# Kernel tuning notes

Hardware: AMD Instinct MI355X
Metric: run time of the kernel (lower is better)

The kernel has to match this reference:

```python
import jax, jax.numpy as jnp
import numpy as np

T, H, W = 4, 16, 16
S = T * H * W          # 1024 flattened sequence length
C = 576                # embd_dim
NH = 8                 # n_head
DK = C // NH           # 72 per-head dim
L = 4                  # n_layer
B = 4                  # batch
PD = C // 3            # 192 per-axis pos-embed dim


def setup_inputs() -> dict:
    key = jax.random.key(0)
    ks = jax.random.split(key, 10)
    s = 1.0 / np.sqrt(C)
    return {
        "x": jax.random.normal(ks[0], (B, T, H, W, C), jnp.float32),
        "pos0": jax.random.normal(ks[1], (T, PD), jnp.float32) * 0.01,
        "pos1": jax.random.normal(ks[2], (H, PD), jnp.float32) * 0.01,
        "pos2": jax.random.normal(ks[3], (W, PD), jnp.float32) * 0.01,
        "ln1_g": jnp.ones((L, C), jnp.float32),
        "ln1_b": jnp.zeros((L, C), jnp.float32),
        "wq": jax.random.normal(ks[4], (L, C, C), jnp.float32) * s,
        "wk": jax.random.normal(ks[5], (L, C, C), jnp.float32) * s,
        "wv": jax.random.normal(ks[6], (L, C, C), jnp.float32) * s,
        "wo": jax.random.normal(ks[7], (L, C, C), jnp.float32) * (s / np.sqrt(L)),
        "wo_b": jnp.zeros((L, C), jnp.float32),
        "ln2_g": jnp.ones((L, C), jnp.float32),
        "ln2_b": jnp.zeros((L, C), jnp.float32),
        "w1": jax.random.normal(ks[8], (L, C, 4 * C), jnp.float32) * s,
        "b1": jnp.zeros((L, 4 * C), jnp.float32),
        "w2": jax.random.normal(ks[9], (L, 4 * C, C), jnp.float32) * (s / 2.0),
        "b2": jnp.zeros((L, C), jnp.float32),
    }


def _layernorm(x, g, b):
    # Faithful to the source: float32 math, and (1e-5 + rsqrt(var)) multiplier
    # (note: source adds eps to rsqrt, not to var -- replicated exactly).
    xf = x.astype(jnp.float32)
    mu = xf.mean(-1, keepdims=True)
    var = jnp.mean(jnp.square(xf - mu), -1, keepdims=True)
    y = (xf - mu) * (1e-5 + jax.lax.rsqrt(var)) * g + b
    return y.astype(x.dtype)


def _stack(x, pos0, pos1, pos2, ln1_g, ln1_b, wq, wk, wv, wo, wo_b,
           ln2_g, ln2_b, w1, b1, w2, b2):
    b = x.shape[0]
    xf = x.reshape(b, S, C)
    # right_shift (decode_step=None): shift flattened tokens right by one
    xf = jnp.pad(xf[:, :-1], ((0, 0), (1, 0), (0, 0)))
    # broadcast positional embedding, concat along channel
    pos = jnp.concatenate([
        jnp.broadcast_to(pos0[:, None, None, :], (T, H, W, PD)),
        jnp.broadcast_to(pos1[None, :, None, :], (T, H, W, PD)),
        jnp.broadcast_to(pos2[None, None, :, :], (T, H, W, PD)),
    ], axis=-1).reshape(S, C)
    xf = xf + pos

    causal = jnp.tril(jnp.ones((S, S), bool))
    scale = 1.0 / np.sqrt(DK)
    neg_inf = jnp.float32(-jnp.inf)

    for l in range(L):  # fixed small layer loop
        # --- causal full self-attention ---
        h = _layernorm(xf, ln1_g[l], ln1_b[l])
        q = (h @ wq[l]).reshape(b, S, NH, DK).transpose(0, 2, 1, 3)
        k = (h @ wk[l]).reshape(b, S, NH, DK).transpose(0, 2, 1, 3)
        v = (h @ wv[l]).reshape(b, S, NH, DK).transpose(0, 2, 1, 3)
        att = jnp.einsum('bhqd,bhkd->bhqk', q, k) * scale
        att = jnp.where(causal, att, neg_inf)
        att = jax.nn.softmax(att, axis=-1)
        a = jnp.einsum('bhqk,bhkd->bhqd', att, v)
        a = a.transpose(0, 2, 1, 3).reshape(b, S, C)
        xf = xf + a @ wo[l] + wo_b[l]
        # --- FFN with GeLU2: sigmoid(1.702*x)*x ---
        h = _layernorm(xf, ln2_g[l], ln2_b[l])
        h = h @ w1[l] + b1[l]
        h = jax.nn.sigmoid(1.702 * h) * h
        xf = xf + h @ w2[l] + b2[l]
    return xf.reshape(b, T, H, W, C)


def reference(x, pos0, pos1, pos2, ln1_g, ln1_b, wq, wk, wv, wo, wo_b,
              ln2_g, ln2_b, w1, b1, w2, b2):
    return _stack(x, pos0, pos1, pos2, ln1_g, ln1_b, wq, wk, wv, wo, wo_b,
                  ln2_g, ln2_b, w1, b1, w2, b2)
```

## Files before the change

### kernel.cpp

```cpp
#include <hip/hip_runtime.h>
#include <hip/hip_bf16.h>

typedef __hip_bfloat16 bf16;
using bf16x8 = __attribute__((ext_vector_type(8))) short;
using f32x4  = __attribute__((ext_vector_type(4))) float;

#define S_LEN 1024
#define CDIM  576
#define NHEAD 8
#define DKH   72
#define BATCH 4
#define MROWS 4096
#define FFDIM 2304
#define QKVN  1728

__device__ __forceinline__ void gload16(const void* g, void* l) {
  __builtin_amdgcn_global_load_lds(
      (const __attribute__((address_space(1))) unsigned int*)g,
      (__attribute__((address_space(3))) unsigned int*)l, 16, 0, 0);
}

__device__ __forceinline__ short f2bf_bits(float x) {
  unsigned int u = __float_as_uint(x);
  u += 0x7fffu + ((u >> 16) & 1u);
  return (short)(u >> 16);
}

__global__ __launch_bounds__(256) void transpose_cvt(
    const float* __restrict__ in, bf16* __restrict__ out, int K, int N,
    size_t in_ls, size_t out_ls) {
  __shared__ float tile[32][33];
  const float* inl = in + (size_t)blockIdx.z * in_ls;
  bf16* outl = out + (size_t)blockIdx.z * out_ls;
  int n0 = blockIdx.x * 32, k0 = blockIdx.y * 32;
  int tx = threadIdx.x & 31, ty = threadIdx.x >> 5;
#pragma unroll
  for (int i = 0; i < 32; i += 8)
    tile[ty + i][tx] = inl[(size_t)(k0 + ty + i) * N + (n0 + tx)];
  __syncthreads();
#pragma unroll
  for (int i = 0; i < 32; i += 8)
    outl[(size_t)(n0 + ty + i) * K + (k0 + tx)] = __float2bfloat16(tile[tx][ty + i]);
}

__global__ __launch_bounds__(256) void build_xf(
    const float* __restrict__ x, const float* __restrict__ p0,
    const float* __restrict__ p1, const float* __restrict__ p2,
    float* __restrict__ xf) {
  int idx = blockIdx.x * 256 + threadIdx.x;
  int c4 = idx % 144;
  int s  = (idx / 144) & (S_LEN - 1);
  int b  = idx / (144 * S_LEN);
  int c  = c4 * 4;
  int t = s >> 8, hh = (s >> 4) & 15, w = s & 15;
  float4 pv;
  if (c < 192)       pv = *(const float4*)&p0[t  * 192 + c];
  else if (c < 384)  pv = *(const float4*)&p1[hh * 192 + c - 192];
  else               pv = *(const float4*)&p2[w  * 192 + c - 384];
  float4 xv = make_float4(0.f, 0.f, 0.f, 0.f);
  if (s > 0) xv = *(const float4*)&x[((size_t)b * S_LEN + s - 1) * CDIM + c];
  float4 r = make_float4(xv.x + pv.x, xv.y + pv.y, xv.z + pv.z, xv.w + pv.w);
  *(float4*)&xf[((size_t)b * S_LEN + s) * CDIM + c] = r;
}

__global__ __launch_bounds__(256) void ln_kernel(
    const float* __restrict__ x, const float* __restrict__ g,
    const float* __restrict__ b, bf16* __restrict__ out) {
  int row  = blockIdx.x * 4 + (threadIdx.x >> 6);
  int lane = threadIdx.x & 63;
  const float* xr = x + (size_t)row * CDIM;
  float vals[9];
  float sum = 0.f;
#pragma unroll
  for (int i = 0; i < 9; i++) { vals[i] = xr[lane + 64 * i]; sum += vals[i]; }
#pragma unroll
  for (int o = 1; o < 64; o <<= 1) sum += __shfl_xor(sum, o);
  float mu = sum * (1.f / CDIM);
  float vs = 0.f;
#pragma unroll
  for (int i = 0; i < 9; i++) { float d = vals[i] - mu; vs += d * d; }
#pragma unroll
  for (int o = 1; o < 64; o <<= 1) vs += __shfl_xor(vs, o);
  float mult = 1e-5f + rsqrtf(vs * (1.f / CDIM));
  bf16* orow = out + (size_t)row * CDIM;
#pragma unroll
  for (int i = 0; i < 9; i++) {
    int c = lane + 64 * i;
    orow[c] = __float2bfloat16((vals[i] - mu) * mult * g[c] + b[c]);
  }
}

template <int BM, bool BIAS, bool RES, int ACT, bool OUTBF>
__global__ __launch_bounds__(256) void gemm3(
    const bf16* __restrict__ A, const bf16* __restrict__ Bt,
    const float* __restrict__ bias, const float* __restrict__ res,
    void* __restrict__ outp, int N, int K) {
  constexpr int MI = BM / 32;
  __shared__ short ldsA[BM][44];
  __shared__ short ldsB[64][44];
  const int tid = threadIdx.x, lane = tid & 63, wave = tid >> 6;
  const int lr = lane & 15, quad = lane >> 4;
  const int m0 = blockIdx.x * BM, n0 = blockIdx.y * 64;
  const int wm = (wave & 1) * (BM / 2), wn = (wave >> 1) * 32;
  f32x4 acc[MI][2] = {};
  const int arow = (BM == 128) ? (tid >> 1) : (tid >> 2);
  const int acol = (BM == 128) ? ((tid & 1) * 16) : ((tid & 3) * 8);
  const int brow = tid >> 2, bcol = (tid & 3) * 8;
  const short* Ag = (const short*)A  + (size_t)(m0 + arow) * K + acol;
  const short* Bg = (const short*)Bt + (size_t)(n0 + brow) * K + bcol;

  for (int k0 = 0; k0 < K; k0 += 32) {
    bf16x8 av0 = *(const bf16x8*)(Ag + k0);
    bf16x8 av1;
    if (BM == 128) av1 = *(const bf16x8*)(Ag + k0 + 8);
    bf16x8 bv = *(const bf16x8*)(Bg + k0);
    *(bf16x8*)&ldsA[arow][acol] = av0;
    if (BM == 128) *(bf16x8*)&ldsA[arow][acol + 8] = av1;
    *(bf16x8*)&ldsB[brow][bcol] = bv;
    __syncthreads();
    bf16x8 af[MI], bfv[2];
#pragma unroll
    for (int mi = 0; mi < MI; mi++)
      af[mi] = *(const bf16x8*)&ldsA[wm + mi * 16 + lr][quad * 8];
#pragma unroll
    for (int ni = 0; ni < 2; ni++)
      bfv[ni] = *(const bf16x8*)&ldsB[wn + ni * 16 + lr][quad * 8];
#pragma unroll
    for (int mi = 0; mi < MI; mi++)
#pragma unroll
      for (int ni = 0; ni < 2; ni++)
        acc[mi][ni] = __builtin_amdgcn_mfma_f32_16x16x32_bf16(af[mi], bfv[ni], acc[mi][ni], 0, 0, 0);
    __syncthreads();
  }

  float* fout = (float*)outp;
  bf16*  bout = (bf16*)outp;
#pragma unroll
  for (int mi = 0; mi < MI; mi++)
#pragma unroll
    for (int ni = 0; ni < 2; ni++) {
      int col = n0 + wn + ni * 16 + lr;
#pragma unroll
      for (int r = 0; r < 4; r++) {
        int row = m0 + wm + mi * 16 + quad * 4 + r;
        float v = acc[mi][ni][r];
        if (BIAS) v += bias[col];
        if (ACT == 1) v = v / (1.f + __expf(-1.702f * v));
        size_t idx = (size_t)row * N + col;
        if (RES) v += res[idx];
        if (OUTBF) bout[idx] = __float2bfloat16(v);
        else       fout[idx] = v;
      }
    }
}

__global__ __launch_bounds__(256) void attn_mfma(
    const bf16* __restrict__ qkv, bf16* __restrict__ a) {
  __shared__ short ldsK[12 * 512];
  __shared__ short ldsVt[80][104];
  __shared__ short ldsP[4 * 1024];
  const int bh = blockIdx.y, b = bh >> 3, h = bh & 7;
  const int tid = threadIdx.x, wave = tid >> 6, lane = tid & 63;
  const int lr = lane & 15, quad = lane >> 4;
  const int qt = 15 - (int)blockIdx.x;
  const float scale = 0.11785113019775793f;
  const int qcol = h * DKH, kcol = CDIM + h * DKH, vcol = 2 * CDIM + h * DKH;

  const int qrow = qt * 64 + wave * 16 + lr;
  const short* qg = (const short*)qkv + (size_t)(b * S_LEN + qrow) * QKVN + qcol;
  bf16x8 qfrag[3];
#pragma unroll
  for (int c = 0; c < 3; c++) {
    int d0 = c * 32 + quad * 8;
    bf16x8 z = {0, 0, 0, 0, 0, 0, 0, 0};
    qfrag[c] = (d0 < DKH) ? *(const bf16x8*)(qg + d0) : z;
  }
  f32x4 oacc[5] = {};
  float m[4], l[4];
#pragma unroll
  for (int r = 0; r < 4; r++) { m[r] = -1e30f; l[r] = 0.f; }

  for (int kt = 0; kt <= qt; kt++) {
    __syncthreads();
    {
      const short* kg = (const short*)qkv +
          (size_t)(b * S_LEN + kt * 64 + wave * 16 + lr) * QKVN + kcol + quad * 8;
#pragma unroll
      for (int c = 0; c < 3; c++)
        gload16(kg + c * 32, &ldsK[(wave * 3 + c) * 512]);
    }
    {
      int key = tid & 63, dgb = tid >> 6;
      const short* vg = (const short*)qkv + (size_t)(b * S_LEN + kt * 64 + key) * QKVN + vcol;
#pragma unroll
      for (int pass = 0; pass < 3; pass++) {
        int d0 = (dgb + pass * 4) * 8;
        if (d0 < 80) {
          bf16x8 vv = {0, 0, 0, 0, 0, 0, 0, 0};
          if (d0 < DKH) vv = *(const bf16x8*)(vg + d0);
#pragma unroll
          for (int j = 0; j < 8; j++) ldsVt[d0 + j][key] = vv[j];
        }
      }
    }
    __syncthreads();
    f32x4 sacc[4] = {};
#pragma unroll
    for (int nc = 0; nc < 4; nc++)
#pragma unroll
      for (int c = 0; c < 3; c++) {
        bf16x8 kf = *(const bf16x8*)&ldsK[(nc * 3 + c) * 512 + lane * 8];
        sacc[nc] = __builtin_amdgcn_mfma_f32_16x16x32_bf16(qfrag[c], kf, sacc[nc], 0, 0, 0);
      }
    float tmax[4];
#pragma unroll
    for (int r = 0; r < 4; r++) tmax[r] = -1e30f;
    bool diag = (kt == qt);
#pragma unroll
    for (int nc = 0; nc < 4; nc++)
#pragma unroll
      for (int r = 0; r < 4; r++) {
        float s = sacc[nc][r] * scale;
        if (diag && (nc * 16 + lr > wave * 16 + quad * 4 + r)) s = -1e30f;
        sacc[nc][r] = s;
        tmax[r] = fmaxf(tmax[r], s);
      }
#pragma unroll
    for (int r = 0; r < 4; r++) {
      tmax[r] = fmaxf(tmax[r], __shfl_xor(tmax[r], 1));
      tmax[r] = fmaxf(tmax[r], __shfl_xor(tmax[r], 2));
      tmax[r] = fmaxf(tmax[r], __shfl_xor(tmax[r], 4));
      tmax[r] = fmaxf(tmax[r], __shfl_xor(tmax[r], 8));
    }
    float alpha[4], psum[4];
#pragma unroll
    for (int r = 0; r < 4; r++) {
      float mn = fmaxf(m[r], tmax[r]);
      alpha[r] = __expf(m[r] - mn);
      m[r] = mn;
      psum[r] = 0.f;
    }
#pragma unroll
    for (int nc = 0; nc < 4; nc++)
#pragma unroll
      for (int r = 0; r < 4; r++) {
        float p = __expf(sacc[nc][r] - m[r]);
        psum[r] += p;
        int col = nc * 16 + lr;
        ldsP[wave * 1024 + (col >> 5) * 512 +
             (((col >> 3) & 3) * 16 + quad * 4 + r) * 8 + (col & 7)] = f2bf_bits(p);
      }
#pragma unroll
    for (int r = 0; r < 4; r++) {
      psum[r] += __shfl_xor(psum[r], 1);
      psum[r] += __shfl_xor(psum[r], 2);
      psum[r] += __shfl_xor(psum[r], 4);
      psum[r] += __shfl_xor(psum[r], 8);
      l[r] = l[r] * alpha[r] + psum[r];
    }
#pragma unroll
    for (int dc = 0; dc < 5; dc++)
#pragma unroll
      for (int r = 0; r < 4; r++) oacc[dc][r] *= alpha[r];
    __builtin_amdgcn_sched_barrier(0);
    bf16x8 pfrag[2];
#pragma unroll
    for (int kc = 0; kc < 2; kc++)
      pfrag[kc] = *(const bf16x8*)&ldsP[wave * 1024 + kc * 512 + lane * 8];
#pragma unroll
    for (int dc = 0; dc < 5; dc++)
#pragma unroll
      for (int kc = 0; kc < 2; kc++) {
        bf16x8 vf = *(const bf16x8*)&ldsVt[dc * 16 + lr][kc * 32 + quad * 8];
        oacc[dc] = __builtin_amdgcn_mfma_f32_16x16x32_bf16(pfrag[kc], vf, oacc[dc], 0, 0, 0);
      }
  }

#pragma unroll
  for (int dc = 0; dc < 5; dc++) {
    int d = dc * 16 + lr;
    if (d < DKH) {
#pragma unroll
      for (int r = 0; r < 4; r++) {
        int row = qt * 64 + wave * 16 + quad * 4 + r;
        float val = oacc[dc][r] / l[r];
        a[(size_t)(b * S_LEN + row) * CDIM + h * DKH + d] = __float2bfloat16(val);
      }
    }
  }
}

extern "C" void kernel_launch(void* const* d_in, const int* in_sizes, int n_in,
                              void* d_out, int out_size, void* d_ws, size_t ws_size,
                              hipStream_t stream) {
  const float* x    = (const float*)d_in[0];
  const float* pos0 = (const float*)d_in[1];
  const float* pos1 = (const float*)d_in[2];
  const float* pos2 = (const float*)d_in[3];
  const float* ln1g = (const float*)d_in[4];
  const float* ln1b = (const float*)d_in[5];
  const float* wq   = (const float*)d_in[6];
  const float* wk   = (const float*)d_in[7];
  const float* wv   = (const float*)d_in[8];
  const float* wo   = (const float*)d_in[9];
  const float* wob  = (const float*)d_in[10];
  const float* ln2g = (const float*)d_in[11];
  const float* ln2b = (const float*)d_in[12];
  const float* w1   = (const float*)d_in[13];
  const float* b1   = (const float*)d_in[14];
  const float* w2   = (const float*)d_in[15];
  const float* b2   = (const float*)d_in[16];

  char* ws = (char*)d_ws;
  size_t off = 0;
  auto alloc = [&](size_t bytes) {
    char* p = ws + off;
    off += (bytes + 255) & ~(size_t)255;
    return p;
  };
  bf16* wqkvT = (bf16*)alloc((size_t)4 * QKVN * CDIM * sizeof(bf16));
  bf16* woT   = (bf16*)alloc((size_t)4 * CDIM * CDIM * sizeof(bf16));
  bf16* w1T   = (bf16*)alloc((size_t)4 * FFDIM * CDIM * sizeof(bf16));
  bf16* w2T   = (bf16*)alloc((size_t)4 * CDIM * FFDIM * sizeof(bf16));
  bf16* hbuf  = (bf16*)alloc((size_t)MROWS * CDIM * sizeof(bf16));
  bf16* abuf  = (bf16*)alloc((size_t)MROWS * CDIM * sizeof(bf16));
  bf16* ubuf  = (bf16*)alloc((size_t)MROWS * FFDIM * sizeof(bf16));
  bf16* qkvb  = (bf16*)alloc((size_t)MROWS * QKVN * sizeof(bf16));
  float* xf   = (float*)d_out;

  const size_t ils  = (size_t)CDIM * CDIM;
  const size_t ils2 = (size_t)CDIM * FFDIM;
  const size_t qkv_ls = (size_t)QKVN * CDIM;
  transpose_cvt<<<dim3(18, 18, 4), 256, 0, stream>>>(wq, wqkvT, CDIM, CDIM, ils, qkv_ls);
  transpose_cvt<<<dim3(18, 18, 4), 256, 0, stream>>>(wk, wqkvT + (size_t)CDIM * CDIM, CDIM, CDIM, ils, qkv_ls);
  transpose_cvt<<<dim3(18, 18, 4), 256, 0, stream>>>(wv, wqkvT + (size_t)2 * CDIM * CDIM, CDIM, CDIM, ils, qkv_ls);
  transpose_cvt<<<dim3(18, 18, 4), 256, 0, stream>>>(wo, woT, CDIM, CDIM, ils, ils);
  transpose_cvt<<<dim3(72, 18, 4), 256, 0, stream>>>(w1, w1T, CDIM, FFDIM, ils2, ils2);
  transpose_cvt<<<dim3(18, 72, 4), 256, 0, stream>>>(w2, w2T, FFDIM, CDIM, ils2, ils2);

  build_xf<<<2304, 256, 0, stream>>>(x, pos0, pos1, pos2, xf);

  for (int l = 0; l < 4; l++) {
    bf16* wqkv_l = wqkvT + (size_t)l * qkv_ls;
    bf16* wo_l   = woT   + (size_t)l * ils;
    bf16* w1_l   = w1T   + (size_t)l * ils2;
    bf16* w2_l   = w2T   + (size_t)l * ils2;

    ln_kernel<<<1024, 256, 0, stream>>>(xf, ln1g + l * CDIM, ln1b + l * CDIM, hbuf);
    gemm3<128, false, false, 0, true><<<dim3(32, QKVN / 64), 256, 0, stream>>>(
        hbuf, wqkv_l, nullptr, nullptr, qkvb, QKVN, CDIM);
    attn_mfma<<<dim3(16, 32), 256, 0, stream>>>(qkvb, abuf);
    gemm3<64, true, true, 0, false><<<dim3(64, CDIM / 64), 256, 0, stream>>>(
        abuf, wo_l, wob + l * CDIM, xf, xf, CDIM, CDIM);
    ln_kernel<<<1024, 256, 0, stream>>>(xf, ln2g + l * CDIM, ln2b + l * CDIM, hbuf);
    gemm3<128, true, false, 1, true><<<dim3(32, FFDIM / 64), 256, 0, stream>>>(
        hbuf, w1_l, b1 + l * FFDIM, nullptr, ubuf, FFDIM, CDIM);
    gemm3<64, true, true, 0, false><<<dim3(64, CDIM / 64), 256, 0, stream>>>(
        ubuf, w2_l, b2 + l * CDIM, xf, xf, CDIM, FFDIM);
  }
}
```

Baseline: 805.3 us.

## Double-buffer GEMM with split-K atomics and pretransposed V for attention

Replaces the GEMM with a 64x64 tile kernel that uses register-staged double-buffered LDS, a 64-wide K step and MFMA-fragment-ordered LDS layout. The Wo and W2 projections now use split-K with atomicAdd into the residual stream, which adds blocks for these narrow GEMMs. A new kernel pre-transposes V per head so attention can load V tiles with direct global-to-LDS loads instead of scalar scattered LDS writes. The costs are an extra kernel launch per layer and float atomics, which make the summation order nondeterministic.

```diff
diff --git a/kernel.cpp b/kernel.cpp
--- a/kernel.cpp
+++ b/kernel.cpp
@@ -13,6 +13,8 @@
 #define MROWS 4096
 #define FFDIM 2304
 #define QKVN  1728
+#define VT_D  80
+#define VT_LS (VT_D * S_LEN)
 
 __device__ __forceinline__ void gload16(const void* g, void* l) {
   __builtin_amdgcn_global_load_lds(
@@ -41,6 +43,29 @@
 #pragma unroll
   for (int i = 0; i < 32; i += 8)
     outl[(size_t)(n0 + ty + i) * K + (k0 + tx)] = __float2bfloat16(tile[tx][ty + i]);
+}
+
+__global__ __launch_bounds__(256) void vt_kernel(
+    const bf16* __restrict__ qkvb, bf16* __restrict__ vT) {
+  __shared__ short tile[32][33];
+  int bh = blockIdx.z, b = bh >> 3, h = bh & 7;
+  int s0 = blockIdx.x * 32, d0 = blockIdx.y * 32;
+  int tx = threadIdx.x & 31, ty = threadIdx.x >> 5;
+  const short* src = (const short*)qkvb;
+  short* dst = (short*)vT + (size_t)bh * VT_LS;
+#pragma unroll
+  for (int i = 0; i < 32; i += 8) {
+    int s = s0 + ty + i, dh = d0 + tx;
+    short v = 0;
+    if (dh < DKH) v = src[(size_t)(b * S_LEN + s) * QKVN + 2 * CDIM + h * DKH + dh];
+    tile[ty + i][tx] = v;
+  }
+  __syncthreads();
+#pragma unroll
+  for (int i = 0; i < 32; i += 8) {
+    int dh = d0 + ty + i, s = s0 + tx;
+    if (dh < VT_D) dst[(size_t)dh * S_LEN + s] = tile[tx][ty + i];
+  }
 }
 
 __global__ __launch_bounds__(256) void build_xf(
@@ -90,81 +115,98 @@
   }
 }
 
-template <int BM, bool BIAS, bool RES, int ACT, bool OUTBF>
-__global__ __launch_bounds__(256) void gemm3(
+template <int SPLITK, bool BIAS, int ACT, bool OUTBF>
+__global__ __launch_bounds__(256) void gemm5(
     const bf16* __restrict__ A, const bf16* __restrict__ Bt,
-    const float* __restrict__ bias, const float* __restrict__ res,
-    void* __restrict__ outp, int N, int K) {
-  constexpr int MI = BM / 32;
-  __shared__ short ldsA[BM][44];
-  __shared__ short ldsB[64][44];
+    const float* __restrict__ bias, void* __restrict__ outp,
+    int N, int Ktot) {
+  const int Ks = Ktot / SPLITK;
+  const int kbase = (SPLITK > 1) ? blockIdx.z * Ks : 0;
+  __shared__ short ldsA[2][2][4][512];
+  __shared__ short ldsB[2][2][4][512];
   const int tid = threadIdx.x, lane = tid & 63, wave = tid >> 6;
   const int lr = lane & 15, quad = lane >> 4;
-  const int m0 = blockIdx.x * BM, n0 = blockIdx.y * 64;
-  const int wm = (wave & 1) * (BM / 2), wn = (wave >> 1) * 32;
-  f32x4 acc[MI][2] = {};
-  const int arow = (BM == 128) ? (tid >> 1) : (tid >> 2);
-  const int acol = (BM == 128) ? ((tid & 1) * 16) : ((tid & 3) * 8);
-  const int brow = tid >> 2, bcol = (tid & 3) * 8;
-  const short* Ag = (const short*)A  + (size_t)(m0 + arow) * K + acol;
-  const short* Bg = (const short*)Bt + (size_t)(n0 + brow) * K + bcol;
-
-  for (int k0 = 0; k0 < K; k0 += 32) {
-    bf16x8 av0 = *(const bf16x8*)(Ag + k0);
-    bf16x8 av1;
-    if (BM == 128) av1 = *(const bf16x8*)(Ag + k0 + 8);
-    bf16x8 bv = *(const bf16x8*)(Bg + k0);
-    *(bf16x8*)&ldsA[arow][acol] = av0;
-    if (BM == 128) *(bf16x8*)&ldsA[arow][acol + 8] = av1;
-    *(bf16x8*)&ldsB[brow][bcol] = bv;
-    __syncthreads();
-    bf16x8 af[MI], bfv[2];
-#pragma unroll
-    for (int mi = 0; mi < MI; mi++)
-      af[mi] = *(const bf16x8*)&ldsA[wm + mi * 16 + lr][quad * 8];
-#pragma unroll
-    for (int ni = 0; ni < 2; ni++)
-      bfv[ni] = *(const bf16x8*)&ldsB[wn + ni * 16 + lr][quad * 8];
-#pragma unroll
-    for (int mi = 0; mi < MI; mi++)
+  const int m0 = blockIdx.x * 64, n0 = blockIdx.y * 64;
+  const int srow = wave * 16 + (tid & 15);
+  const int skc  = ((tid >> 4) & 3) * 8;
+  const short* Ag = (const short*)A  + (size_t)(m0 + srow) * Ktot + kbase + skc;
+  const short* Bg = (const short*)Bt + (size_t)(n0 + srow) * Ktot + kbase + skc;
+  const int loff = lane * 8;
+  f32x4 acc[2][2] = {};
+
+  *(bf16x8*)&ldsA[0][0][wave][loff] = *(const bf16x8*)(Ag);
+  *(bf16x8*)&ldsA[0][1][wave][loff] = *(const bf16x8*)(Ag + 32);
+  *(bf16x8*)&ldsB[0][0][wave][loff] = *(const bf16x8*)(Bg);
+  *(bf16x8*)&ldsB[0][1][wave][loff] = *(const bf16x8*)(Bg + 32);
+  __syncthreads();
+
+  int buf = 0;
+  for (int k0 = 0; k0 < Ks; k0 += 64, buf ^= 1) {
+    const bool more = (k0 + 64) < Ks;
+    bf16x8 na0, na1, nb0, nb1;
+    if (more) {
+      na0 = *(const bf16x8*)(Ag + k0 + 64);
+      na1 = *(const bf16x8*)(Ag + k0 + 96);
+      nb0 = *(const bf16x8*)(Bg + k0 + 64);
+      nb1 = *(const bf16x8*)(Bg + k0 + 96);
+    }
+#pragma unroll
+    for (int kc = 0; kc < 2; kc++) {
+      bf16x8 af[2], bfv[2];
+#pragma unroll
+      for (int mi = 0; mi < 2; mi++)
+        af[mi] = *(const bf16x8*)&ldsA[buf][kc][(wave & 1) * 2 + mi][loff];
 #pragma unroll
       for (int ni = 0; ni < 2; ni++)
-        acc[mi][ni] = __builtin_amdgcn_mfma_f32_16x16x32_bf16(af[mi], bfv[ni], acc[mi][ni], 0, 0, 0);
+        bfv[ni] = *(const bf16x8*)&ldsB[buf][kc][(wave >> 1) * 2 + ni][loff];
+#pragma unroll
+      for (int mi = 0; mi < 2; mi++)
+#pragma unroll
+        for (int ni = 0; ni < 2; ni++)
+          acc[mi][ni] = __builtin_amdgcn_mfma_f32_16x16x32_bf16(af[mi], bfv[ni], acc[mi][ni], 0, 0, 0);
+    }
+    if (more) {
+      *(bf16x8*)&ldsA[buf ^ 1][0][wave][loff] = na0;
+      *(bf16x8*)&ldsA[buf ^ 1][1][wave][loff] = na1;
+      *(bf16x8*)&ldsB[buf ^ 1][0][wave][loff] = nb0;
+      *(bf16x8*)&ldsB[buf ^ 1][1][wave][loff] = nb1;
+    }
     __syncthreads();
   }
 
   float* fout = (float*)outp;
   bf16*  bout = (bf16*)outp;
 #pragma unroll
-  for (int mi = 0; mi < MI; mi++)
+  for (int mi = 0; mi < 2; mi++)
 #pragma unroll
     for (int ni = 0; ni < 2; ni++) {
-      int col = n0 + wn + ni * 16 + lr;
+      int col = n0 + (wave >> 1) * 32 + ni * 16 + lr;
 #pragma unroll
       for (int r = 0; r < 4; r++) {
-        int row = m0 + wm + mi * 16 + quad * 4 + r;
+        int row = m0 + (wave & 1) * 32 + mi * 16 + quad * 4 + r;
         float v = acc[mi][ni][r];
-        if (BIAS) v += bias[col];
+        if (BIAS && (SPLITK == 1 || blockIdx.z == 0)) v += bias[col];
         if (ACT == 1) v = v / (1.f + __expf(-1.702f * v));
         size_t idx = (size_t)row * N + col;
-        if (RES) v += res[idx];
-        if (OUTBF) bout[idx] = __float2bfloat16(v);
-        else       fout[idx] = v;
+        if (SPLITK > 1)      atomicAdd(&fout[idx], v);
+        else if (OUTBF)      bout[idx] = __float2bfloat16(v);
+        else                 fout[idx] = v;
       }
     }
 }
 
 __global__ __launch_bounds__(256) void attn_mfma(
-    const bf16* __restrict__ qkv, bf16* __restrict__ a) {
+    const bf16* __restrict__ qkv, const bf16* __restrict__ vT,
+    bf16* __restrict__ a) {
   __shared__ short ldsK[12 * 512];
-  __shared__ short ldsVt[80][104];
+  __shared__ short ldsV[10 * 512];
   __shared__ short ldsP[4 * 1024];
   const int bh = blockIdx.y, b = bh >> 3, h = bh & 7;
   const int tid = threadIdx.x, wave = tid >> 6, lane = tid & 63;
   const int lr = lane & 15, quad = lane >> 4;
   const int qt = 15 - (int)blockIdx.x;
   const float scale = 0.11785113019775793f;
-  const int qcol = h * DKH, kcol = CDIM + h * DKH, vcol = 2 * CDIM + h * DKH;
+  const int qcol = h * DKH, kcol = CDIM + h * DKH;
 
   const int qrow = qt * 64 + wave * 16 + lr;
   const short* qg = (const short*)qkv + (size_t)(b * S_LEN + qrow) * QKVN + qcol;
@@ -179,6 +221,8 @@
   float m[4], l[4];
 #pragma unroll
   for (int r = 0; r < 4; r++) { m[r] = -1e30f; l[r] = 0.f; }
+
+  const short* vtb = (const short*)vT + (size_t)bh * VT_LS;
 
   for (int kt = 0; kt <= qt; kt++) {
     __syncthreads();
@@ -189,19 +233,11 @@
       for (int c = 0; c < 3; c++)
         gload16(kg + c * 32, &ldsK[(wave * 3 + c) * 512]);
     }
-    {
-      int key = tid & 63, dgb = tid >> 6;
-      const short* vg = (const short*)qkv + (size_t)(b * S_LEN + kt * 64 + key) * QKVN + vcol;
-#pragma unroll
-      for (int pass = 0; pass < 3; pass++) {
-        int d0 = (dgb + pass * 4) * 8;
-        if (d0 < 80) {
-          bf16x8 vv = {0, 0, 0, 0, 0, 0, 0, 0};
-          if (d0 < DKH) vv = *(const bf16x8*)(vg + d0);
-#pragma unroll
-          for (int j = 0; j < 8; j++) ldsVt[d0 + j][key] = vv[j];
-        }
-      }
+#pragma unroll
+    for (int p = wave; p < 10; p += 4) {
+      int dc = p >> 1, kc = p & 1;
+      const short* vg = vtb + (size_t)(dc * 16 + lr) * S_LEN + kt * 64 + kc * 32 + quad * 8;
+      gload16(vg, &ldsV[p * 512]);
     }
     __syncthreads();
     f32x4 sacc[4] = {};
@@ -271,7 +307,7 @@
     for (int dc = 0; dc < 5; dc++)
 #pragma unroll
       for (int kc = 0; kc < 2; kc++) {
-        bf16x8 vf = *(const bf16x8*)&ldsVt[dc * 16 + lr][kc * 32 + quad * 8];
+        bf16x8 vf = *(const bf16x8*)&ldsV[(dc * 2 + kc) * 512 + lane * 8];
         oacc[dc] = __builtin_amdgcn_mfma_f32_16x16x32_bf16(pfrag[kc], vf, oacc[dc], 0, 0, 0);
       }
   }
@@ -318,22 +354,23 @@
     off += (bytes + 255) & ~(size_t)255;
     return p;
   };
-  bf16* wqkvT = (bf16*)alloc((size_t)4 * QKVN * CDIM * sizeof(bf16));
-  bf16* woT   = (bf16*)alloc((size_t)4 * CDIM * CDIM * sizeof(bf16));
-  bf16* w1T   = (bf16*)alloc((size_t)4 * FFDIM * CDIM * sizeof(bf16));
-  bf16* w2T   = (bf16*)alloc((size_t)4 * CDIM * FFDIM * sizeof(bf16));
+  const size_t ils  = (size_t)CDIM * CDIM;
+  const size_t ils2 = (size_t)CDIM * FFDIM;
+  const size_t qkv_ls = (size_t)QKVN * CDIM;
+  bf16* wqkvT = (bf16*)alloc(4 * qkv_ls * sizeof(bf16));
+  bf16* woT   = (bf16*)alloc(4 * ils * sizeof(bf16));
+  bf16* w1T   = (bf16*)alloc(4 * ils2 * sizeof(bf16));
+  bf16* w2T   = (bf16*)alloc(4 * ils2 * sizeof(bf16));
   bf16* hbuf  = (bf16*)alloc((size_t)MROWS * CDIM * sizeof(bf16));
   bf16* abuf  = (bf16*)alloc((size_t)MROWS * CDIM * sizeof(bf16));
   bf16* ubuf  = (bf16*)alloc((size_t)MROWS * FFDIM * sizeof(bf16));
   bf16* qkvb  = (bf16*)alloc((size_t)MROWS * QKVN * sizeof(bf16));
+  bf16* vTb   = (bf16*)alloc((size_t)32 * VT_LS * sizeof(bf16));
   float* xf   = (float*)d_out;
 
-  const size_t ils  = (size_t)CDIM * CDIM;
-  const size_t ils2 = (size_t)CDIM * FFDIM;
-  const size_t qkv_ls = (size_t)QKVN * CDIM;
   transpose_cvt<<<dim3(18, 18, 4), 256, 0, stream>>>(wq, wqkvT, CDIM, CDIM, ils, qkv_ls);
-  transpose_cvt<<<dim3(18, 18, 4), 256, 0, stream>>>(wk, wqkvT + (size_t)CDIM * CDIM, CDIM, CDIM, ils, qkv_ls);
-  transpose_cvt<<<dim3(18, 18, 4), 256, 0, stream>>>(wv, wqkvT + (size_t)2 * CDIM * CDIM, CDIM, CDIM, ils, qkv_ls);
+  transpose_cvt<<<dim3(18, 18, 4), 256, 0, stream>>>(wk, wqkvT + ils, CDIM, CDIM, ils, qkv_ls);
+  transpose_cvt<<<dim3(18, 18, 4), 256, 0, stream>>>(wv, wqkvT + 2 * ils, CDIM, CDIM, ils, qkv_ls);
   transpose_cvt<<<dim3(18, 18, 4), 256, 0, stream>>>(wo, woT, CDIM, CDIM, ils, ils);
   transpose_cvt<<<dim3(72, 18, 4), 256, 0, stream>>>(w1, w1T, CDIM, FFDIM, ils2, ils2);
   transpose_cvt<<<dim3(18, 72, 4), 256, 0, stream>>>(w2, w2T, FFDIM, CDIM, ils2, ils2);
@@ -347,15 +384,16 @@
     bf16* w2_l   = w2T   + (size_t)l * ils2;
 
     ln_kernel<<<1024, 256, 0, stream>>>(xf, ln1g + l * CDIM, ln1b + l * CDIM, hbuf);
-    gemm3<128, false, false, 0, true><<<dim3(32, QKVN / 64), 256, 0, stream>>>(
-        hbuf, wqkv_l, nullptr, nullptr, qkvb, QKVN, CDIM);
-    attn_mfma<<<dim3(16, 32), 256, 0, stream>>>(qkvb, abuf);
-    gemm3<64, true, true, 0, false><<<dim3(64, CDIM / 64), 256, 0, stream>>>(
-        abuf, wo_l, wob + l * CDIM, xf, xf, CDIM, CDIM);
+    gemm5<1, false, 0, true><<<dim3(64, 27, 1), 256, 0, stream>>>(
+        hbuf, wqkv_l, nullptr, qkvb, QKVN, CDIM);
+    vt_kernel<<<dim3(32, 3, 32), 256, 0, stream>>>(qkvb, vTb);
+    attn_mfma<<<dim3(16, 32), 256, 0, stream>>>(qkvb, vTb, abuf);
+    gemm5<3, true, 0, false><<<dim3(64, 9, 3), 256, 0, stream>>>(
+        abuf, wo_l, wob + l * CDIM, xf, CDIM, CDIM);
     ln_kernel<<<1024, 256, 0, stream>>>(xf, ln2g + l * CDIM, ln2b + l * CDIM, hbuf);
-    gemm3<128, true, false, 1, true><<<dim3(32, FFDIM / 64), 256, 0, stream>>>(
-        hbuf, w1_l, b1 + l * FFDIM, nullptr, ubuf, FFDIM, CDIM);
-    gemm3<64, true, true, 0, false><<<dim3(64, CDIM / 64), 256, 0, stream>>>(
-        ubuf, w2_l, b2 + l * CDIM, xf, xf, CDIM, FFDIM);
-  }
-}
+    gemm5<1, true, 1, true><<<dim3(64, 36, 1), 256, 0, stream>>>(
+        hbuf, w1_l, b1 + l * FFDIM, ubuf, FFDIM, CDIM);
+    gemm5<4, true, 0, false><<<dim3(64, 9, 4), 256, 0, stream>>>(
+        ubuf, w2_l, b2 + l * CDIM, xf, CDIM, FFDIM);
+  }
+}
```

Result: slower. 1.007 ms (+25.0%).
